# Performance work log

Hardware: AMD Instinct MI355X
Metric: run time of the kernel (lower is better)

The kernel has to match this reference:

```python
import jax, jax.numpy as jnp
import numpy as np

C_IN = 256
NUM_CLASSES = 19
NUM_PROTO = 10
LN_EPS = 1e-5
L2_EPS = 1e-12


def l2_normalize(x):
    # matches F.normalize(x, p=2, dim=-1): divide by max(norm, eps)
    n = jnp.linalg.norm(x, axis=-1, keepdims=True)
    return x / jnp.maximum(n, L2_EPS)


def layer_norm(x, g, b):
    mu = jnp.mean(x, axis=-1, keepdims=True)
    var = jnp.mean(jnp.square(x - mu), axis=-1, keepdims=True)
    return (x - mu) * jax.lax.rsqrt(var + LN_EPS) * g + b


def setup_inputs() -> dict:
    key = jax.random.key(0)
    ks = jax.random.split(key, 8)
    B, H, W = 8, 128, 128
    x = jax.random.normal(ks[0], (B, C_IN, H, W), dtype=jnp.float32)
    # ProjectionHead: Conv2d(256,256,1) -> ReLU -> Conv2d(256,256,1); 1x1 convs as matrices [out,in]
    w1 = jax.random.normal(ks[1], (C_IN, C_IN), dtype=jnp.float32) * 0.02
    b1 = jnp.zeros((C_IN,), dtype=jnp.float32)
    w2 = jax.random.normal(ks[2], (C_IN, C_IN), dtype=jnp.float32) * 0.02
    b2 = jnp.zeros((C_IN,), dtype=jnp.float32)
    # feat_norm = LayerNorm(256), mask_norm = LayerNorm(num_classes)
    ln1_g = jnp.ones((C_IN,), dtype=jnp.float32)
    ln1_b = jnp.zeros((C_IN,), dtype=jnp.float32)
    ln2_g = jnp.ones((NUM_CLASSES,), dtype=jnp.float32)
    ln2_b = jnp.zeros((NUM_CLASSES,), dtype=jnp.float32)
    # prototypes: trunc_normal(std=0.02), [K, M, D]
    prototypes = jax.random.truncated_normal(ks[3], -2.0, 2.0, (NUM_CLASSES, NUM_PROTO, C_IN), dtype=jnp.float32) * 0.02
    return {"x": x, "w1": w1, "b1": b1, "w2": w2, "b2": b2,
            "ln1_g": ln1_g, "ln1_b": ln1_b, "ln2_g": ln2_g, "ln2_b": ln2_b,
            "prototypes": prototypes, "out_h": 512, "out_w": 512}


def reference(x, w1, b1, w2, b2, ln1_g, ln1_b, ln2_g, ln2_b, prototypes, out_h, out_w):
    B, _, H, W = x.shape
    # ProjectionHead: 1x1 conv -> relu -> 1x1 conv, then F.normalize(dim=-1)
    h = jnp.einsum('bchw,oc->bohw', x, w1) + b1[None, :, None, None]
    h = jax.nn.relu(h)
    h = jnp.einsum('bchw,oc->bohw', h, w2) + b2[None, :, None, None]
    h = l2_normalize(h)  # faithful: torch normalizes along last axis (W) of BCHW here
    # (b h w) c
    _c = jnp.transpose(h, (0, 2, 3, 1)).reshape(-1, C_IN)
    _c = layer_norm(_c, ln1_g, ln1_b)
    _c = l2_normalize(_c)
    protos = l2_normalize(prototypes)  # prototypes.data.copy_(l2_normalize(prototypes))
    # cosine similarity against all class prototypes: [n, m, k]
    masks = jnp.einsum('nd,kmd->nmk', _c, protos)
    out_seg = jnp.max(masks, axis=1)          # amax over prototypes -> [n, k]
    out_seg = layer_norm(out_seg, ln2_g, ln2_b)
    out_seg = out_seg.reshape(B, H, W, NUM_CLASSES).transpose(0, 3, 1, 2)
    out_seg = jax.image.resize(out_seg, (B, NUM_CLASSES, out_h, out_w), method='cubic')
    return out_seg
```

## Files before the change

### kernel.cpp

```cpp
#include <hip/hip_runtime.h>
#include <hip/hip_fp16.h>


typedef _Float16 f16;
typedef _Float16 f16x4 __attribute__((ext_vector_type(4)));
typedef _Float16 f16x8 __attribute__((ext_vector_type(8)));
typedef float    f32x16 __attribute__((ext_vector_type(16)));

#define HW2   16384
#define NCLS  19

__device__ __forceinline__ int swz128(int row, int b) {
  return row*128 + ((((b >> 4) ^ (row & 7)) << 4) | (b & 15));
}
__device__ __forceinline__ int swz512(int row, int b) {
  return row*512 + ((((b >> 4) ^ (row & 31)) << 4) | (b & 15));
}

__device__ __forceinline__ void stage128(const char* __restrict__ g, char* lds,
                                         long gstride, int niter, int wid, int nw, int lane) {
  int rin = lane >> 3, s = lane & 7;
  for (int i = wid; i < niter; i += nw) {
    int r = i*8 + rin;
    uint4 v = *(const uint4*)(g + (long)r*gstride + s*16);
    *(uint4*)(lds + r*128 + ((s ^ (r & 7)) << 4)) = v;
  }
}

__global__ void k_prep(const float* __restrict__ w1, const float* __restrict__ w2,
                       const float* __restrict__ protos,
                       f16* __restrict__ w1h, f16* __restrict__ w2h, f16* __restrict__ prth)
{
  int b = blockIdx.x, l = threadIdx.x;
  if (b < 512) {
    const float* src = (b < 256) ? (w1 + (size_t)b*256) : (w2 + (size_t)(b-256)*256);
    f16* dst = (b < 256) ? (w1h + (size_t)b*256) : (w2h + (size_t)(b-256)*256);
    #pragma unroll
    for (int j = 0; j < 4; ++j) dst[l + 64*j] = (f16)src[l + 64*j];
  } else {
    int r = b - 512;
    if (r < 190) {
      float v[4]; float s = 0.f;
      #pragma unroll
      for (int j = 0; j < 4; ++j) { v[j] = protos[(size_t)r*256 + l + 64*j]; s += v[j]*v[j]; }
      #pragma unroll
      for (int m = 1; m < 64; m <<= 1) s += __shfl_xor(s, m);
      float sc = 1.f / fmaxf(sqrtf(s), 1e-12f);
      #pragma unroll
      for (int j = 0; j < 4; ++j) prth[(size_t)r*256 + l + 64*j] = (f16)(v[j]*sc);
    } else {
      #pragma unroll
      for (int j = 0; j < 4; ++j) prth[(size_t)r*256 + l + 64*j] = (f16)0.f;
    }
  }
}

__global__ void __launch_bounds__(512, 1) k_fused(
    const float* __restrict__ xf,
    const f16* __restrict__ w1h, const float* __restrict__ b1g,
    const f16* __restrict__ w2h, const float* __restrict__ b2g,
    const float* __restrict__ ln1g, const float* __restrict__ ln1b,
    const f16* __restrict__ prth, const float* __restrict__ ln2g, const float* __restrict__ ln2b,
    float* __restrict__ outs)
{
  __shared__ char smem[114688];
  char* As = smem;
  char* Bs = smem + 16384;
  char* H  = smem + 49152;
  float* nbuf = (float*)smem;
  float* Lg   = (float*)(smem + 4096);
  float* Lb   = (float*)(smem + 5120);
  float* Os   = (float*)(smem + 98304);

  int bid = blockIdx.x;
  int b = bid >> 7, pt = bid & 127;
  int tid = threadIdx.x, lane = tid & 63, wid = tid >> 6;
  int hi = lane >> 5, l31 = lane & 31;
  int wp = wid >> 2, wn = wid & 3;

  f32x16 acc[2][2];
  #pragma unroll
  for (int m = 0; m < 2; ++m)
    #pragma unroll
    for (int n = 0; n < 2; ++n)
      #pragma unroll
      for (int r = 0; r < 16; ++r) acc[m][n][r] = 0.f;

  for (int cc = 0; cc < 4; ++cc) {
    __syncthreads();
    {
      int cg = tid >> 5, pg = tid & 31;
      const float* xb = xf + ((size_t)(b*256 + cc*64 + cg*4))*HW2 + pt*128 + pg*4;
      float4 v0 = *(const float4*)(xb);
      float4 v1 = *(const float4*)(xb + HW2);
      float4 v2 = *(const float4*)(xb + 2*HW2);
      float4 v3 = *(const float4*)(xb + 3*HW2);
      #define PUT(rr, c0, c1, c2, c3) { f16x4 h4 = { (f16)(c0), (f16)(c1), (f16)(c2), (f16)(c3) }; \
        *(f16x4*)(As + swz128(pg*4 + rr, cg*8)) = h4; }
      PUT(0, v0.x, v1.x, v2.x, v3.x)
      PUT(1, v0.y, v1.y, v2.y, v3.y)
      PUT(2, v0.z, v1.z, v2.z, v3.z)
      PUT(3, v0.w, v1.w, v2.w, v3.w)
      #undef PUT
    }
    stage128((const char*)w1h + cc*128, Bs, 512, 32, wid, 8, lane);
    __syncthreads();
    #pragma unroll
    for (int kk = 0; kk < 4; ++kk) {
      int byteK = kk*32 + hi*16;
      f16x8 a0 = *(const f16x8*)(As + swz128(wp*64 +      l31, byteK));
      f16x8 a1 = *(const f16x8*)(As + swz128(wp*64 + 32 + l31, byteK));
      f16x8 b0 = *(const f16x8*)(Bs + swz128(wn*64 +      l31, byteK));
      f16x8 b1 = *(const f16x8*)(Bs + swz128(wn*64 + 32 + l31, byteK));
      acc[0][0] = __builtin_amdgcn_mfma_f32_32x32x16_f16(a0, b0, acc[0][0], 0, 0, 0);
      acc[0][1] = __builtin_amdgcn_mfma_f32_32x32x16_f16(a0, b1, acc[0][1], 0, 0, 0);
      acc[1][0] = __builtin_amdgcn_mfma_f32_32x32x16_f16(a1, b0, acc[1][0], 0, 0, 0);
      acc[1][1] = __builtin_amdgcn_mfma_f32_32x32x16_f16(a1, b1, acc[1][1], 0, 0, 0);
    }
  }
  __syncthreads();
  #pragma unroll
  for (int n = 0; n < 2; ++n) {
    int o = wn*64 + n*32 + l31;
    float bv = b1g[o];
    #pragma unroll
    for (int m = 0; m < 2; ++m)
      #pragma unroll
      for (int r = 0; r < 16; ++r) {
        int p = wp*64 + m*32 + (r & 3) + 8*(r >> 2) + 4*hi;
        *(f16*)(H + swz512(p, o*2)) = (f16)fmaxf(acc[m][n][r] + bv, 0.f);
      }
  }

  #pragma unroll
  for (int m = 0; m < 2; ++m)
    #pragma unroll
    for (int n = 0; n < 2; ++n)
      #pragma unroll
      for (int r = 0; r < 16; ++r) acc[m][n][r] = 0.f;

  for (int cc = 0; cc < 4; ++cc) {
    __syncthreads();
    stage128((const char*)w2h + cc*128, Bs, 512, 32, wid, 8, lane);
    __syncthreads();
    #pragma unroll
    for (int kk = 0; kk < 4; ++kk) {
      int byteC = cc*128 + kk*32 + hi*16;
      int byteK = kk*32 + hi*16;
      f16x8 a0 = *(const f16x8*)(H + swz512(wp*64 +      l31, byteC));
      f16x8 a1 = *(const f16x8*)(H + swz512(wp*64 + 32 + l31, byteC));
      f16x8 b0 = *(const f16x8*)(Bs + swz128(wn*64 +      l31, byteK));
      f16x8 b1 = *(const f16x8*)(Bs + swz128(wn*64 + 32 + l31, byteK));
      acc[0][0] = __builtin_amdgcn_mfma_f32_32x32x16_f16(a0, b0, acc[0][0], 0, 0, 0);
      acc[0][1] = __builtin_amdgcn_mfma_f32_32x32x16_f16(a0, b1, acc[0][1], 0, 0, 0);
      acc[1][0] = __builtin_amdgcn_mfma_f32_32x32x16_f16(a1, b0, acc[1][0], 0, 0, 0);
      acc[1][1] = __builtin_amdgcn_mfma_f32_32x32x16_f16(a1, b1, acc[1][1], 0, 0, 0);
    }
  }
  __syncthreads();

  float sn[2];
  #pragma unroll
  for (int n = 0; n < 2; ++n) {
    int o = wn*64 + n*32 + l31;
    float bv = b2g[o];
    float s = 0.f;
    #pragma unroll
    for (int m = 0; m < 2; ++m)
      #pragma unroll
      for (int r = 0; r < 16; ++r) { acc[m][n][r] += bv; s += acc[m][n][r]*acc[m][n][r]; }
    s += __shfl_xor(s, 32);
    sn[n] = s;
  }
  if (lane < 32) {
    nbuf[wp*256 + wn*64 +      lane] = sn[0];
    nbuf[wp*256 + wn*64 + 32 + lane] = sn[1];
  }
  if (tid < 256) { Lg[tid] = ln1g[tid]; Lb[tid] = ln1b[tid]; }
  __syncthreads();
  #pragma unroll
  for (int n = 0; n < 2; ++n) {
    int o = wn*64 + n*32 + l31;
    float tot = nbuf[o] + nbuf[256 + o];
    float sc = 1.f / fmaxf(sqrtf(tot), 1e-12f);
    #pragma unroll
    for (int m = 0; m < 2; ++m)
      #pragma unroll
      for (int r = 0; r < 16; ++r) {
        int p = wp*64 + m*32 + (r & 3) + 8*(r >> 2) + 4*hi;
        *(f16*)(H + swz512(p, o*2)) = (f16)(acc[m][n][r]*sc);
      }
  }
  __syncthreads();

  {
    int p = tid >> 2, q = tid & 3;
    f16x8 hreg[8];
    float sh = 0.f;
    #pragma unroll
    for (int j = 0; j < 8; ++j) {
      hreg[j] = *(const f16x8*)(H + swz512(p, q*128 + j*16));
      #pragma unroll
      for (int e = 0; e < 8; ++e) sh += (float)hreg[j][e];
    }
    sh += __shfl_xor(sh, 1); sh += __shfl_xor(sh, 2);
    float mu = sh * (1.f/256.f);
    float sv = 0.f;
    #pragma unroll
    for (int j = 0; j < 8; ++j)
      #pragma unroll
      for (int e = 0; e < 8; ++e) { float d = (float)hreg[j][e] - mu; sv += d*d; }
    sv += __shfl_xor(sv, 1); sv += __shfl_xor(sv, 2);
    float rstd = rsqrtf(sv*(1.f/256.f) + 1e-5f);
    float s2 = 0.f; f16x8 creg[8];
    #pragma unroll
    for (int j = 0; j < 8; ++j) {
      int ob = q*64 + j*8;
      #pragma unroll
      for (int e = 0; e < 8; ++e) {
        float c = ((float)hreg[j][e] - mu)*rstd*Lg[ob+e] + Lb[ob+e];
        s2 += c*c; creg[j][e] = (f16)c;
      }
    }
    s2 += __shfl_xor(s2, 1); s2 += __shfl_xor(s2, 2);
    float scale = 1.f / fmaxf(sqrtf(s2), 1e-12f);
    #pragma unroll
    for (int j = 0; j < 8; ++j) {
      f16x8 w;
      #pragma unroll
      for (int e = 0; e < 8; ++e) w[e] = (f16)((float)creg[j][e]*scale);
      *(f16x8*)(H + swz512(p, q*128 + j*16)) = w;
    }
  }

  int wj = wid & 1, wp2 = wid >> 1;
  f32x16 am[3];
  #pragma unroll
  for (int n = 0; n < 3; ++n)
    #pragma unroll
    for (int r = 0; r < 16; ++r) am[n][r] = 0.f;

  for (int cci = 0; cci < 4; ++cci) {
    __syncthreads();
    stage128((const char*)prth + cci*128, Bs, 512, 24, wid, 8, lane);
    __syncthreads();
    #pragma unroll
    for (int kk = 0; kk < 4; ++kk) {
      int byteC = cci*128 + kk*32 + hi*16;
      int byteK = kk*32 + hi*16;
      f16x8 af = *(const f16x8*)(H + swz512(wp2*32 + l31, byteC));
      #pragma unroll
      for (int n = 0; n < 3; ++n) {
        f16x8 bf = *(const f16x8*)(Bs + swz128(wj*96 + n*32 + l31, byteK));
        am[n] = __builtin_amdgcn_mfma_f32_32x32x16_f16(af, bf, am[n], 0, 0, 0);
      }
    }
  }
  __syncthreads();

  #pragma unroll
  for (int n = 0; n < 3; ++n) {
    int j = wj*96 + n*32 + l31;
    #pragma unroll
    for (int r = 0; r < 16; ++r) {
      int p = wp2*32 + (r & 3) + 8*(r >> 2) + 4*hi;
      *(float*)(smem + swz512(j, p*4)) = am[n][r];
    }
  }
  __syncthreads();

  {
    int pp = tid >> 2, ql = tid & 3;
    float mx[5]; float ssum = 0.f;
    #pragma unroll
    for (int ki = 0; ki < 5; ++ki) {
      int k = ql + 4*ki;
      float m = 0.f;
      if (k < NCLS) {
        m = -1e30f;
        #pragma unroll
        for (int mm = 0; mm < 10; ++mm)
          m = fmaxf(m, *(const float*)(smem + swz512(k*10 + mm, pp*4)));
        ssum += m;
      }
      mx[ki] = m;
    }
    ssum += __shfl_xor(ssum, 1); ssum += __shfl_xor(ssum, 2);
    float mu2 = ssum * (1.f/19.f);
    float sv2 = 0.f;
    #pragma unroll
    for (int ki = 0; ki < 5; ++ki) {
      int k = ql + 4*ki;
      if (k < NCLS) { float d = mx[ki]-mu2; sv2 += d*d; }
    }
    sv2 += __shfl_xor(sv2, 1); sv2 += __shfl_xor(sv2, 2);
    float rstd2 = rsqrtf(sv2*(1.f/19.f) + 1e-5f);
    #pragma unroll
    for (int ki = 0; ki < 5; ++ki) {
      int k = ql + 4*ki;
      if (k < NCLS) Os[k*128 + pp] = (mx[ki]-mu2)*rstd2*ln2g[k] + ln2b[k];
    }
  }
  __syncthreads();
  for (int idx = tid; idx < NCLS*128; idx += 512) {
    int k = idx >> 7, pp = idx & 127;
    outs[((size_t)b*NCLS + k)*HW2 + pt*128 + pp] = Os[idx];
  }
}

__device__ __forceinline__ float kcub(float t) {
  if (t >= 2.f) return 0.f;
  if (t >= 1.f) return ((-0.5f*t + 2.5f)*t - 4.f)*t + 2.f;
  return ((1.5f*t - 2.5f)*t)*t + 1.f;
}

__global__ void __launch_bounds__(256) k_resize(const float* __restrict__ outs,
                                                float* __restrict__ out)
{
  int ch = blockIdx.x >> 3, slab = blockIdx.x & 7;
  const float* src = outs + (size_t)ch*HW2;
  float* dst = out + (size_t)ch*262144;
  __shared__ float rows[20*128];
  __shared__ float wyt[64][4];
  int tid = threadIdx.x;

  int r0 = slab*16 - 2; if (r0 < 0) r0 = 0;
  int r1 = slab*16 + 17; if (r1 > 127) r1 = 127;
  int nr = r1 - r0 + 1;
  for (int idx = tid; idx < nr*128; idx += 256) rows[idx] = src[r0*128 + idx];

  if (tid < 64) {
    int y = slab*64 + tid;
    float s = y*0.25f - 0.375f;
    float jf = floorf(s); int j = (int)jf; float f = s - jf;
    float w[4] = { kcub(1.f+f), kcub(f), kcub(1.f-f), kcub(2.f-f) };
    float ws = 0.f;
    #pragma unroll
    for (int k = 0; k < 4; ++k) { int t = j-1+k; if (t < 0 || t > 127) w[k] = 0.f; ws += w[k]; }
    float inv = 1.f/ws;
    #pragma unroll
    for (int k = 0; k < 4; ++k) wyt[tid][k] = w[k]*inv;
  }
  __syncthreads();

  float wx[2][4]; int tx[2][4];
  #pragma unroll
  for (int cI = 0; cI < 2; ++cI) {
    int xc = tid + cI*256;
    float s = xc*0.25f - 0.375f;
    float jf = floorf(s); int j = (int)jf; float f = s - jf;
    float w[4] = { kcub(1.f+f), kcub(f), kcub(1.f-f), kcub(2.f-f) };
    float ws = 0.f;
    #pragma unroll
    for (int k = 0; k < 4; ++k) { int t = j-1+k; if (t < 0 || t > 127) w[k] = 0.f; ws += w[k]; }
    #pragma unroll
    for (int k = 0; k < 4; ++k) {
      wx[cI][k] = w[k]/ws;
      int t = j-1+k; tx[cI][k] = t < 0 ? 0 : (t > 127 ? 127 : t);
    }
  }

  auto rowdot = [&](int cI, int absrow) -> float {
    int rr = absrow < 0 ? 0 : (absrow > 127 ? 127 : absrow);
    const float* rp = rows + (rr - r0)*128;
    return wx[cI][0]*rp[tx[cI][0]] + wx[cI][1]*rp[tx[cI][1]]
         + wx[cI][2]*rp[tx[cI][2]] + wx[cI][3]*rp[tx[cI][3]];
  };

  int base = slab*16;
  float a0 = rowdot(0, base-2), a1 = rowdot(0, base-1), a2 = rowdot(0, base),   a3 = rowdot(0, base+1);
  float b0 = rowdot(1, base-2), b1 = rowdot(1, base-1), b2 = rowdot(1, base),   b3 = rowdot(1, base+1);

  for (int m = 0; m < 16; ++m) {
    float na  = rowdot(0, base + m + 2);
    float nb2 = rowdot(1, base + m + 2);
    int y0 = m*4;
    {
      float w0 = wyt[y0][0],   w1 = wyt[y0][1],   w2 = wyt[y0][2],   w3 = wyt[y0][3];
      size_t ob = ((size_t)(slab*64 + y0))*512;
      dst[ob + tid]       = w0*a0 + w1*a1 + w2*a2 + w3*a3;
      dst[ob + tid + 256] = w0*b0 + w1*b1 + w2*b2 + w3*b3;
    }
    {
      float w0 = wyt[y0+1][0], w1 = wyt[y0+1][1], w2 = wyt[y0+1][2], w3 = wyt[y0+1][3];
      size_t ob = ((size_t)(slab*64 + y0 + 1))*512;
      dst[ob + tid]       = w0*a0 + w1*a1 + w2*a2 + w3*a3;
      dst[ob + tid + 256] = w0*b0 + w1*b1 + w2*b2 + w3*b3;
    }
    {
      float w0 = wyt[y0+2][0], w1 = wyt[y0+2][1], w2 = wyt[y0+2][2], w3 = wyt[y0+2][3];
      size_t ob = ((size_t)(slab*64 + y0 + 2))*512;
      dst[ob + tid]       = w0*a1 + w1*a2 + w2*a3 + w3*na;
      dst[ob + tid + 256] = w0*b1 + w1*b2 + w2*b3 + w3*nb2;
    }
    {
      float w0 = wyt[y0+3][0], w1 = wyt[y0+3][1], w2 = wyt[y0+3][2], w3 = wyt[y0+3][3];
      size_t ob = ((size_t)(slab*64 + y0 + 3))*512;
      dst[ob + tid]       = w0*a1 + w1*a2 + w2*a3 + w3*na;
      dst[ob + tid + 256] = w0*b1 + w1*b2 + w2*b3 + w3*nb2;
    }
    a0 = a1; a1 = a2; a2 = a3; a3 = na;
    b0 = b1; b1 = b2; b2 = b3; b3 = nb2;
  }
}

extern "C" void kernel_launch(void* const* d_in, const int* in_sizes, int n_in,
                              void* d_out, int out_size, void* d_ws, size_t ws_size,
                              hipStream_t stream) {
  (void)in_sizes; (void)n_in; (void)out_size; (void)ws_size;
  const float* x    = (const float*)d_in[0];
  const float* w1   = (const float*)d_in[1];
  const float* b1   = (const float*)d_in[2];
  const float* w2   = (const float*)d_in[3];
  const float* b2   = (const float*)d_in[4];
  const float* ln1g = (const float*)d_in[5];
  const float* ln1b = (const float*)d_in[6];
  const float* ln2g = (const float*)d_in[7];
  const float* ln2b = (const float*)d_in[8];
  const float* prot = (const float*)d_in[9];
  float* out = (float*)d_out;
  char* ws = (char*)d_ws;

  f16*   w1h  = (f16*)(ws + 0);
  f16*   w2h  = (f16*)(ws + 131072);
  f16*   prth = (f16*)(ws + 262144);
  float* outs = (float*)(ws + 360448);

  k_prep  <<<dim3(704),  dim3(64),  0, stream>>>(w1, w2, prot, w1h, w2h, prth);
  k_fused <<<dim3(1024), dim3(512), 0, stream>>>(x, w1h, b1, w2h, b2,
                                                 ln1g, ln1b, prth, ln2g, ln2b, outs);
  k_resize<<<dim3(1216), dim3(256), 0, stream>>>(outs, out);
}
```

Before: 401.5 us.

## Double-buffer weight tiles with direct global-to-LDS loads and prefetch x

```diff
diff --git a/kernel.cpp b/kernel.cpp
--- a/kernel.cpp
+++ b/kernel.cpp
@@ -10,63 +10,70 @@
 #define HW2   16384
 #define NCLS  19
 
-__device__ __forceinline__ int swz128(int row, int b) {
+__device__ __forceinline__ int swzA(int row, int b) {
+  return row*128 + ((((b >> 4) ^ (row & 7) ^ ((row >> 2) & 7)) << 4) | (b & 15));
+}
+__device__ __forceinline__ int swzB(int row, int b) {
   return row*128 + ((((b >> 4) ^ (row & 7)) << 4) | (b & 15));
 }
 __device__ __forceinline__ int swz512(int row, int b) {
   return row*512 + ((((b >> 4) ^ (row & 31)) << 4) | (b & 15));
 }
 
-__device__ __forceinline__ void stage128(const char* __restrict__ g, char* lds,
-                                         long gstride, int niter, int wid, int nw, int lane) {
-  int rin = lane >> 3, s = lane & 7;
-  for (int i = wid; i < niter; i += nw) {
-    int r = i*8 + rin;
-    uint4 v = *(const uint4*)(g + (long)r*gstride + s*16);
-    *(uint4*)(lds + r*128 + ((s ^ (r & 7)) << 4)) = v;
-  }
+__device__ __forceinline__ void gload16(const char* g, char* l) {
+  __builtin_amdgcn_global_load_lds(
+      (const __attribute__((address_space(1))) void*)g,
+      (__attribute__((address_space(3))) void*)l, 16, 0, 0);
 }
 
 __global__ void k_prep(const float* __restrict__ w1, const float* __restrict__ w2,
                        const float* __restrict__ protos,
-                       f16* __restrict__ w1h, f16* __restrict__ w2h, f16* __restrict__ prth)
+                       char* __restrict__ w1i, char* __restrict__ w2i, char* __restrict__ pri)
 {
   int b = blockIdx.x, l = threadIdx.x;
+  int cc = l >> 4, sw = (l >> 1) & 7, tb = (l & 1) * 4;
   if (b < 512) {
-    const float* src = (b < 256) ? (w1 + (size_t)b*256) : (w2 + (size_t)(b-256)*256);
-    f16* dst = (b < 256) ? (w1h + (size_t)b*256) : (w2h + (size_t)(b-256)*256);
-    #pragma unroll
-    for (int j = 0; j < 4; ++j) dst[l + 64*j] = (f16)src[l + 64*j];
+    int o = b & 255;
+    const float* src = (b < 256) ? (w1 + (size_t)o*256) : (w2 + (size_t)o*256);
+    char* img = (b < 256) ? w1i : w2i;
+    int c0 = cc*64 + ((sw ^ (o & 7)) << 3) + tb;
+    float4 v = *(const float4*)(src + c0);
+    f16x4 h = { (f16)v.x, (f16)v.y, (f16)v.z, (f16)v.w };
+    *(f16x4*)(img + cc*32768 + o*128 + sw*16 + tb*2) = h;
   } else {
     int r = b - 512;
+    char* dst = pri + cc*24576 + r*128 + sw*16 + tb*2;
     if (r < 190) {
-      float v[4]; float s = 0.f;
-      #pragma unroll
-      for (int j = 0; j < 4; ++j) { v[j] = protos[(size_t)r*256 + l + 64*j]; s += v[j]*v[j]; }
+      float s = 0.f;
+      #pragma unroll
+      for (int j = 0; j < 4; ++j) { float v = protos[(size_t)r*256 + l + 64*j]; s += v*v; }
       #pragma unroll
       for (int m = 1; m < 64; m <<= 1) s += __shfl_xor(s, m);
       float sc = 1.f / fmaxf(sqrtf(s), 1e-12f);
-      #pragma unroll
-      for (int j = 0; j < 4; ++j) prth[(size_t)r*256 + l + 64*j] = (f16)(v[j]*sc);
+      int c0 = cc*64 + ((sw ^ (r & 7)) << 3) + tb;
+      float4 v = *(const float4*)(protos + (size_t)r*256 + c0);
+      f16x4 h = { (f16)(v.x*sc), (f16)(v.y*sc), (f16)(v.z*sc), (f16)(v.w*sc) };
+      *(f16x4*)dst = h;
     } else {
-      #pragma unroll
-      for (int j = 0; j < 4; ++j) prth[(size_t)r*256 + l + 64*j] = (f16)0.f;
+      f16x4 z = { (f16)0.f, (f16)0.f, (f16)0.f, (f16)0.f };
+      *(f16x4*)dst = z;
     }
   }
 }
 
 __global__ void __launch_bounds__(512, 1) k_fused(
     const float* __restrict__ xf,
-    const f16* __restrict__ w1h, const float* __restrict__ b1g,
-    const f16* __restrict__ w2h, const float* __restrict__ b2g,
+    const char* __restrict__ w1i, const float* __restrict__ b1g,
+    const char* __restrict__ w2i, const float* __restrict__ b2g,
     const float* __restrict__ ln1g, const float* __restrict__ ln1b,
-    const f16* __restrict__ prth, const float* __restrict__ ln2g, const float* __restrict__ ln2b,
+    const char* __restrict__ pri, const float* __restrict__ ln2g, const float* __restrict__ ln2b,
     float* __restrict__ outs)
 {
-  __shared__ char smem[114688];
-  char* As = smem;
-  char* Bs = smem + 16384;
-  char* H  = smem + 49152;
+  __shared__ char smem[147456];
+  char* As  = smem;
+  char* Bs0 = smem + 16384;
+  char* Bs1 = smem + 49152;
+  char* H   = smem + 81920;
   float* nbuf = (float*)smem;
   float* Lg   = (float*)(smem + 4096);
   float* Lb   = (float*)(smem + 5120);
@@ -78,6 +85,20 @@
   int hi = lane >> 5, l31 = lane & 31;
   int wp = wid >> 2, wn = wid & 3;
 
+  int cg = tid >> 5, pg = tid & 31;
+  const float* xbase = xf + (size_t)b*256*HW2 + (size_t)(cg*4)*HW2 + pt*128 + pg*4;
+
+  float4 xr[2][4];
+
+  #pragma unroll
+  for (int i = 0; i < 4; ++i) {
+    int off = wid*4096 + i*1024;
+    gload16(w1i + off + lane*16, Bs0 + off);
+  }
+  #pragma unroll
+  for (int j = 0; j < 4; ++j) xr[0][j] = *(const float4*)(xbase + (size_t)j*HW2);
+  __syncthreads();
+
   f32x16 acc[2][2];
   #pragma unroll
   for (int m = 0; m < 2; ++m)
@@ -86,39 +107,51 @@
       #pragma unroll
       for (int r = 0; r < 16; ++r) acc[m][n][r] = 0.f;
 
+  #pragma unroll
   for (int cc = 0; cc < 4; ++cc) {
-    __syncthreads();
+    char* Bcur = (cc & 1) ? Bs1 : Bs0;
+    char* Bnxt = (cc & 1) ? Bs0 : Bs1;
+    if (cc < 3) {
+      #pragma unroll
+      for (int i = 0; i < 4; ++i) {
+        int off = wid*4096 + i*1024;
+        gload16(w1i + (cc+1)*32768 + off + lane*16, Bnxt + off);
+      }
+      #pragma unroll
+      for (int j = 0; j < 4; ++j)
+        xr[(cc+1)&1][j] = *(const float4*)(xbase + (size_t)((cc+1)*64 + j)*HW2);
+    }
     {
-      int cg = tid >> 5, pg = tid & 31;
-      const float* xb = xf + ((size_t)(b*256 + cc*64 + cg*4))*HW2 + pt*128 + pg*4;
-      float4 v0 = *(const float4*)(xb);
-      float4 v1 = *(const float4*)(xb + HW2);
-      float4 v2 = *(const float4*)(xb + 2*HW2);
-      float4 v3 = *(const float4*)(xb + 3*HW2);
-      #define PUT(rr, c0, c1, c2, c3) { f16x4 h4 = { (f16)(c0), (f16)(c1), (f16)(c2), (f16)(c3) }; \
-        *(f16x4*)(As + swz128(pg*4 + rr, cg*8)) = h4; }
-      PUT(0, v0.x, v1.x, v2.x, v3.x)
-      PUT(1, v0.y, v1.y, v2.y, v3.y)
-      PUT(2, v0.z, v1.z, v2.z, v3.z)
-      PUT(3, v0.w, v1.w, v2.w, v3.w)
-      #undef PUT
-    }
-    stage128((const char*)w1h + cc*128, Bs, 512, 32, wid, 8, lane);
-    __syncthreads();
+      float4 v0 = xr[cc&1][0], v1 = xr[cc&1][1], v2 = xr[cc&1][2], v3 = xr[cc&1][3];
+      f16x4 h;
+      h = f16x4{(f16)v0.x,(f16)v1.x,(f16)v2.x,(f16)v3.x}; *(f16x4*)(As + swzA(pg*4+0, cg*8)) = h;
+      h = f16x4{(f16)v0.y,(f16)v1.y,(f16)v2.y,(f16)v3.y}; *(f16x4*)(As + swzA(pg*4+1, cg*8)) = h;
+      h = f16x4{(f16)v0.z,(f16)v1.z,(f16)v2.z,(f16)v3.z}; *(f16x4*)(As + swzA(pg*4+2, cg*8)) = h;
+      h = f16x4{(f16)v0.w,(f16)v1.w,(f16)v2.w,(f16)v3.w}; *(f16x4*)(As + swzA(pg*4+3, cg*8)) = h;
+    }
+    asm volatile("s_waitcnt lgkmcnt(0)" ::: "memory");
+    __builtin_amdgcn_sched_barrier(0);
+    __builtin_amdgcn_s_barrier();
     #pragma unroll
     for (int kk = 0; kk < 4; ++kk) {
       int byteK = kk*32 + hi*16;
-      f16x8 a0 = *(const f16x8*)(As + swz128(wp*64 +      l31, byteK));
-      f16x8 a1 = *(const f16x8*)(As + swz128(wp*64 + 32 + l31, byteK));
-      f16x8 b0 = *(const f16x8*)(Bs + swz128(wn*64 +      l31, byteK));
-      f16x8 b1 = *(const f16x8*)(Bs + swz128(wn*64 + 32 + l31, byteK));
+      f16x8 a0 = *(const f16x8*)(As + swzA(wp*64 +      l31, byteK));
+      f16x8 a1 = *(const f16x8*)(As + swzA(wp*64 + 32 + l31, byteK));
+      f16x8 b0 = *(const f16x8*)(Bcur + swzB(wn*64 +      l31, byteK));
+      f16x8 b1 = *(const f16x8*)(Bcur + swzB(wn*64 + 32 + l31, byteK));
       acc[0][0] = __builtin_amdgcn_mfma_f32_32x32x16_f16(a0, b0, acc[0][0], 0, 0, 0);
       acc[0][1] = __builtin_amdgcn_mfma_f32_32x32x16_f16(a0, b1, acc[0][1], 0, 0, 0);
       acc[1][0] = __builtin_amdgcn_mfma_f32_32x32x16_f16(a1, b0, acc[1][0], 0, 0, 0);
       acc[1][1] = __builtin_amdgcn_mfma_f32_32x32x16_f16(a1, b1, acc[1][1], 0, 0, 0);
     }
-  }
-  __syncthreads();
+    __syncthreads();
+  }
+
+  #pragma unroll
+  for (int i = 0; i < 4; ++i) {
+    int off = wid*4096 + i*1024;
+    gload16(w2i + off + lane*16, Bs0 + off);
+  }
   #pragma unroll
   for (int n = 0; n < 2; ++n) {
     int o = wn*64 + n*32 + l31;
@@ -131,6 +164,7 @@
         *(f16*)(H + swz512(p, o*2)) = (f16)fmaxf(acc[m][n][r] + bv, 0.f);
       }
   }
+  __syncthreads();
 
   #pragma unroll
   for (int m = 0; m < 2; ++m)
@@ -139,25 +173,38 @@
       #pragma unroll
       for (int r = 0; r < 16; ++r) acc[m][n][r] = 0.f;
 
+  #pragma unroll
   for (int cc = 0; cc < 4; ++cc) {
-    __syncthreads();
-    stage128((const char*)w2h + cc*128, Bs, 512, 32, wid, 8, lane);
-    __syncthreads();
+    char* Bcur = (cc & 1) ? Bs1 : Bs0;
+    char* Bnxt = (cc & 1) ? Bs0 : Bs1;
+    if (cc < 3) {
+      #pragma unroll
+      for (int i = 0; i < 4; ++i) {
+        int off = wid*4096 + i*1024;
+        gload16(w2i + (cc+1)*32768 + off + lane*16, Bnxt + off);
+      }
+    }
     #pragma unroll
     for (int kk = 0; kk < 4; ++kk) {
       int byteC = cc*128 + kk*32 + hi*16;
       int byteK = kk*32 + hi*16;
       f16x8 a0 = *(const f16x8*)(H + swz512(wp*64 +      l31, byteC));
       f16x8 a1 = *(const f16x8*)(H + swz512(wp*64 + 32 + l31, byteC));
-      f16x8 b0 = *(const f16x8*)(Bs + swz128(wn*64 +      l31, byteK));
-      f16x8 b1 = *(const f16x8*)(Bs + swz128(wn*64 + 32 + l31, byteK));
+      f16x8 b0 = *(const f16x8*)(Bcur + swzB(wn*64 +      l31, byteK));
+      f16x8 b1 = *(const f16x8*)(Bcur + swzB(wn*64 + 32 + l31, byteK));
       acc[0][0] = __builtin_amdgcn_mfma_f32_32x32x16_f16(a0, b0, acc[0][0], 0, 0, 0);
       acc[0][1] = __builtin_amdgcn_mfma_f32_32x32x16_f16(a0, b1, acc[0][1], 0, 0, 0);
       acc[1][0] = __builtin_amdgcn_mfma_f32_32x32x16_f16(a1, b0, acc[1][0], 0, 0, 0);
       acc[1][1] = __builtin_amdgcn_mfma_f32_32x32x16_f16(a1, b1, acc[1][1], 0, 0, 0);
     }
-  }
-  __syncthreads();
+    __syncthreads();
+  }
+
+  #pragma unroll
+  for (int i = 0; i < 3; ++i) {
+    int off = wid*3072 + i*1024;
+    gload16(pri + off + lane*16, Bs0 + off);
+  }
 
   float sn[2];
   #pragma unroll
@@ -232,6 +279,7 @@
       *(f16x8*)(H + swz512(p, q*128 + j*16)) = w;
     }
   }
+  __syncthreads();
 
   int wj = wid & 1, wp2 = wid >> 1;
   f32x16 am[3];
@@ -240,10 +288,17 @@
     #pragma unroll
     for (int r = 0; r < 16; ++r) am[n][r] = 0.f;
 
+  #pragma unroll
   for (int cci = 0; cci < 4; ++cci) {
-    __syncthreads();
-    stage128((const char*)prth + cci*128, Bs, 512, 24, wid, 8, lane);
-    __syncthreads();
+    char* Bcur = (cci & 1) ? Bs1 : Bs0;
+    char* Bnxt = (cci & 1) ? Bs0 : Bs1;
+    if (cci < 3) {
+      #pragma unroll
+      for (int i = 0; i < 3; ++i) {
+        int off = wid*3072 + i*1024;
+        gload16(pri + (cci+1)*24576 + off + lane*16, Bnxt + off);
+      }
+    }
     #pragma unroll
     for (int kk = 0; kk < 4; ++kk) {
       int byteC = cci*128 + kk*32 + hi*16;
@@ -251,12 +306,12 @@
       f16x8 af = *(const f16x8*)(H + swz512(wp2*32 + l31, byteC));
       #pragma unroll
       for (int n = 0; n < 3; ++n) {
-        f16x8 bf = *(const f16x8*)(Bs + swz128(wj*96 + n*32 + l31, byteK));
+        f16x8 bf = *(const f16x8*)(Bcur + swzB(wj*96 + n*32 + l31, byteK));
         am[n] = __builtin_amdgcn_mfma_f32_32x32x16_f16(af, bf, am[n], 0, 0, 0);
       }
     }
-  }
-  __syncthreads();
+    __syncthreads();
+  }
 
   #pragma unroll
   for (int n = 0; n < 3; ++n) {
@@ -421,13 +476,13 @@
   float* out = (float*)d_out;
   char* ws = (char*)d_ws;
 
-  f16*   w1h  = (f16*)(ws + 0);
-  f16*   w2h  = (f16*)(ws + 131072);
-  f16*   prth = (f16*)(ws + 262144);
+  char*  w1i  = ws + 0;
+  char*  w2i  = ws + 131072;
+  char*  pri  = ws + 262144;
   float* outs = (float*)(ws + 360448);
 
-  k_prep  <<<dim3(704),  dim3(64),  0, stream>>>(w1, w2, prot, w1h, w2h, prth);
-  k_fused <<<dim3(1024), dim3(512), 0, stream>>>(x, w1h, b1, w2h, b2,
-                                                 ln1g, ln1b, prth, ln2g, ln2b, outs);
+  k_prep  <<<dim3(704),  dim3(64),  0, stream>>>(w1, w2, prot, w1i, w2i, pri);
+  k_fused <<<dim3(1024), dim3(512), 0, stream>>>(x, w1i, b1, w2i, b2,
+                                                 ln1g, ln1b, pri, ln2g, ln2b, outs);
   k_resize<<<dim3(1216), dim3(256), 0, stream>>>(outs, out);
 }
```

Result: faster. 352.7 us (-12.2%).
